# Kernel optimization log

Hardware: AMD Instinct MI355X
Metric: run time of the kernel (lower is better)

Reference implementation:

```python
import jax, jax.numpy as jnp
import numpy as np

B, N, NIN, NH, NOUT = 32, 64, 256, 256, 2
E = N * (N - 1)
BN_EPS = 1e-5


def _xavier(k, fan_in, fan_out):
    return jax.random.normal(k, (fan_in, fan_out), jnp.float32) * np.sqrt(2.0 / (fan_in + fan_out))


def _mlp_params(key, n_in, n_hid, n_out):
    k1, k2 = jax.random.split(key)
    return {
        'w1': _xavier(k1, n_in, n_hid), 'b1': jnp.full((n_hid,), 0.1, jnp.float32),
        'w2': _xavier(k2, n_hid, n_out), 'b2': jnp.full((n_out,), 0.1, jnp.float32),
        'g': jnp.ones((n_out,), jnp.float32), 'beta': jnp.zeros((n_out,), jnp.float32),
    }


def setup_inputs() -> dict:
    key = jax.random.key(0)
    ks = jax.random.split(key, 7)
    inputs = jax.random.normal(ks[0], (B, N, NIN), jnp.float32)
    # fully-connected directed graph w/o self loops: edge e = (send i, recv j), i != j
    idx = np.array([(i, j) for i in range(N) for j in range(N) if i != j], dtype=np.int64)
    rel_send = np.zeros((E, N), np.float32)
    rel_rec = np.zeros((E, N), np.float32)
    rel_send[np.arange(E), idx[:, 0]] = 1.0
    rel_rec[np.arange(E), idx[:, 1]] = 1.0
    out = {'inputs': inputs, 'rel_rec': jnp.asarray(rel_rec), 'rel_send': jnp.asarray(rel_send)}
    for name, (ni, nh, no), k in [('mlp1', (NIN, NH, NH), ks[1]),
                                  ('mlp2', (2 * NH, NH, NH), ks[2]),
                                  ('mlp3', (NH, NH, NH), ks[3]),
                                  ('mlp4', (3 * NH, NH, NH), ks[4])]:
        p = _mlp_params(k, ni, nh, no)
        for pk, pv in p.items():
            out[f'{name}_{pk}'] = pv
    out['fc_w'] = _xavier(ks[5], NH, NOUT)
    out['fc_b'] = jnp.full((NOUT,), 0.1, jnp.float32)
    return out


def _mlp(x, w1, b1, w2, b2, g, beta):
    # Linear -> ELU -> Linear -> ELU -> BatchNorm1d (training-mode batch stats, biased var)
    h = jax.nn.elu(x @ w1 + b1)
    h = jax.nn.elu(h @ w2 + b2)
    mean = h.mean(axis=(0, 1))
    var = h.var(axis=(0, 1))
    return (h - mean) * jax.lax.rsqrt(var + BN_EPS) * g + beta


def reference(inputs, rel_rec, rel_send,
              mlp1_w1, mlp1_b1, mlp1_w2, mlp1_b2, mlp1_g, mlp1_beta,
              mlp2_w1, mlp2_b1, mlp2_w2, mlp2_b2, mlp2_g, mlp2_beta,
              mlp3_w1, mlp3_b1, mlp3_w2, mlp3_b2, mlp3_g, mlp3_beta,
              mlp4_w1, mlp4_b1, mlp4_w2, mlp4_b2, mlp4_g, mlp4_beta,
              fc_w, fc_b):
    x = _mlp(inputs, mlp1_w1, mlp1_b1, mlp1_w2, mlp1_b2, mlp1_g, mlp1_beta)  # [B,N,NH]
    # node2edge: gather sender/receiver node features per edge
    s = jnp.einsum('en,bnh->beh', rel_send, x)
    r = jnp.einsum('en,bnh->beh', rel_rec, x)
    x = jnp.concatenate([s, r], axis=-1)  # [B,E,2*NH]
    x = _mlp(x, mlp2_w1, mlp2_b1, mlp2_w2, mlp2_b2, mlp2_g, mlp2_beta)
    x_skip = x
    # edge2node: scatter-sum incoming edges per node, normalized by N
    inc = jnp.einsum('en,beh->bnh', rel_rec, x) / N
    x = _mlp(inc, mlp3_w1, mlp3_b1, mlp3_w2, mlp3_b2, mlp3_g, mlp3_beta)
    s = jnp.einsum('en,bnh->beh', rel_send, x)
    r = jnp.einsum('en,bnh->beh', rel_rec, x)
    x = jnp.concatenate([s, r, x_skip], axis=-1)  # [B,E,3*NH]
    x = _mlp(x, mlp4_w1, mlp4_b1, mlp4_w2, mlp4_b2, mlp4_g, mlp4_beta)
    return x @ fc_w + fc_b  # [B,E,NOUT]
```

## Files before the change

kernel.cpp:

```cpp
#include <hip/hip_runtime.h>

typedef __bf16 bf16_t;
typedef __bf16 bf16x8 __attribute__((ext_vector_type(8)));
typedef float  f32x4  __attribute__((ext_vector_type(4)));

#define NB    64
#define EB    4032
#define BATCH 32
#define H     256
#define M_EDGE (BATCH*EB)
#define M_NODE (BATCH*NB)
#define T2    4
#define BN_EPS 1e-5f

__device__ __forceinline__ void load_lds16(const void* g, void* l) {
    __builtin_amdgcn_global_load_lds(
        (const __attribute__((address_space(1))) unsigned int*)g,
        (__attribute__((address_space(3))) unsigned int*)l, 16, 0, 0);
}
__device__ __forceinline__ float elu(float v) { return v > 0.f ? v : __expf(v) - 1.f; }

template<bool AF32>
__global__ __launch_bounds__(256)
void fused_mlp(const void* __restrict__ A0v,
               const bf16_t* __restrict__ W1t, const float* __restrict__ b1,
               const bf16_t* __restrict__ W2t, const float* __restrict__ b2,
               bf16_t* __restrict__ out, float* __restrict__ stats)
{
    const int m0 = blockIdx.x * 64;
    const int tid = threadIdx.x, wave = tid >> 6, lane = tid & 63;
    const int l15 = lane & 15, quad = lane >> 4;
    const int row = tid >> 2;
    const int cx8 = (((tid & 3) ^ ((tid >> 3) & 3))) * 8;
    const int sl8 = (tid & 3) * 8;
    const int xq8 = (quad ^ ((l15 >> 1) & 3)) * 8;

    __shared__ bf16_t h1s[64 * 264];
    __shared__ bf16_t Bs[256 * 32];
    __shared__ float  sred[512];

    const bf16_t* A0 = (const bf16_t*)A0v;

    f32x4 acc1[4][4];
#pragma unroll
    for (int t = 0; t < 4; ++t)
#pragma unroll
        for (int u = 0; u < 4; ++u) acc1[t][u] = (f32x4){0.f, 0.f, 0.f, 0.f};

    for (int k0 = 0; k0 < 256; k0 += 32) {
        bf16_t* ldsA = h1s + wave * 512;
        if (AF32) {
            const float* af = (const float*)A0v + (size_t)(m0 + row) * 256 + k0 + cx8;
            float4 lo = *(const float4*)af;
            float4 hi = *(const float4*)(af + 4);
            bf16x8 v;
            v[0]=(bf16_t)lo.x; v[1]=(bf16_t)lo.y; v[2]=(bf16_t)lo.z; v[3]=(bf16_t)lo.w;
            v[4]=(bf16_t)hi.x; v[5]=(bf16_t)hi.y; v[6]=(bf16_t)hi.z; v[7]=(bf16_t)hi.w;
            *(bf16x8*)&h1s[row * 32 + sl8] = v;
        } else {
            load_lds16(A0 + (size_t)(m0 + row) * 256 + k0 + cx8, ldsA);
        }
#pragma unroll
        for (int p = 0; p < 4; ++p)
            load_lds16(W1t + (size_t)(p * 64 + row) * 256 + k0 + cx8,
                       Bs + (p * 256 + wave * 64) * 8);
        __syncthreads();
        bf16x8 afr[4], bfr[4];
#pragma unroll
        for (int t = 0; t < 4; ++t)
            afr[t] = *(const bf16x8*)&h1s[(t * 16 + l15) * 32 + xq8];
#pragma unroll
        for (int u = 0; u < 4; ++u)
            bfr[u] = *(const bf16x8*)&Bs[(wave * 64 + u * 16 + l15) * 32 + xq8];
#pragma unroll
        for (int t = 0; t < 4; ++t)
#pragma unroll
            for (int u = 0; u < 4; ++u)
                acc1[t][u] = __builtin_amdgcn_mfma_f32_16x16x32_bf16(afr[t], bfr[u], acc1[t][u], 0, 0, 0);
        __syncthreads();
    }

#pragma unroll
    for (int u = 0; u < 4; ++u) {
        int   col = wave * 64 + u * 16 + l15;
        float bv  = b1[col];
#pragma unroll
        for (int t = 0; t < 4; ++t)
#pragma unroll
            for (int r = 0; r < 4; ++r)
                h1s[(t * 16 + quad * 4 + r) * 264 + col] = (bf16_t)elu(acc1[t][u][r] + bv);
    }
    sred[tid] = 0.f; sred[256 + tid] = 0.f;
    __syncthreads();

    f32x4 acc2[4][4];
#pragma unroll
    for (int t = 0; t < 4; ++t)
#pragma unroll
        for (int u = 0; u < 4; ++u) acc2[t][u] = (f32x4){0.f, 0.f, 0.f, 0.f};

    for (int k0 = 0; k0 < 256; k0 += 32) {
#pragma unroll
        for (int p = 0; p < 4; ++p)
            load_lds16(W2t + (size_t)(p * 64 + row) * 256 + k0 + cx8,
                       Bs + (p * 256 + wave * 64) * 8);
        __syncthreads();
        bf16x8 afr[4], bfr[4];
#pragma unroll
        for (int t = 0; t < 4; ++t)
            afr[t] = *(const bf16x8*)&h1s[(t * 16 + l15) * 264 + k0 + quad * 8];
#pragma unroll
        for (int u = 0; u < 4; ++u)
            bfr[u] = *(const bf16x8*)&Bs[(wave * 64 + u * 16 + l15) * 32 + xq8];
#pragma unroll
        for (int t = 0; t < 4; ++t)
#pragma unroll
            for (int u = 0; u < 4; ++u)
                acc2[t][u] = __builtin_amdgcn_mfma_f32_16x16x32_bf16(afr[t], bfr[u], acc2[t][u], 0, 0, 0);
        __syncthreads();
    }

#pragma unroll
    for (int u = 0; u < 4; ++u) {
        int   col = wave * 64 + u * 16 + l15;
        float bv  = b2[col];
        float s = 0.f, q = 0.f;
#pragma unroll
        for (int t = 0; t < 4; ++t)
#pragma unroll
            for (int r = 0; r < 4; ++r) {
                float v = elu(acc2[t][u][r] + bv);
                h1s[(t * 16 + quad * 4 + r) * 264 + col] = (bf16_t)v;
                s += v; q += v * v;
            }
        s += __shfl_xor(s, 16); s += __shfl_xor(s, 32);
        q += __shfl_xor(q, 16); q += __shfl_xor(q, 32);
        if (quad == 0) { atomicAdd(&sred[col], s); atomicAdd(&sred[256 + col], q); }
    }
    __syncthreads();
#pragma unroll
    for (int p = 0; p < 8; ++p) {
        int idx = p * 256 + tid;
        int r = idx >> 5, ch = idx & 31;
        *(uint4*)&out[(size_t)(m0 + r) * H + ch * 8] = *(const uint4*)&h1s[r * 264 + ch * 8];
    }
    atomicAdd(&stats[tid],     sred[tid]);
    atomicAdd(&stats[H + tid], sred[256 + tid]);
}

__global__ __launch_bounds__(256)
void node_gemm(const bf16_t* __restrict__ A, const float* __restrict__ statsIn,
               const float* __restrict__ g, const float* __restrict__ beta, float Mcnt,
               const bf16_t* __restrict__ Wt, const float* __restrict__ bias,
               float* __restrict__ out)
{
    const int m0 = blockIdx.x * 64;
    const int nb = blockIdx.y * 256;
    const int tid = threadIdx.x, wave = tid >> 6, lane = tid & 63;
    const int l15 = lane & 15, quad = lane >> 4;
    const int row = tid >> 2;
    const int cx8 = (((tid & 3) ^ ((tid >> 3) & 3))) * 8;
    const int sl8 = (tid & 3) * 8;
    const int xq8 = (quad ^ ((l15 >> 1) & 3)) * 8;
    __shared__ bf16_t As[64 * 32];
    __shared__ bf16_t Bs[256 * 32];
    __shared__ float  ss[512];

    {
        float mean = statsIn[tid] / Mcnt;
        float var  = statsIn[256 + tid] / Mcnt - mean * mean;
        float scl  = g[tid] * rsqrtf(var + BN_EPS);
        ss[tid]       = scl;
        ss[256 + tid] = beta[tid] - mean * scl;
    }
    __syncthreads();

    f32x4 acc[4][4];
#pragma unroll
    for (int t = 0; t < 4; ++t)
#pragma unroll
        for (int u = 0; u < 4; ++u) acc[t][u] = (f32x4){0.f, 0.f, 0.f, 0.f};

    for (int k0 = 0; k0 < 256; k0 += 32) {
        {
            int kc = k0 + cx8;
            bf16x8 v = *(const bf16x8*)(A + (size_t)(m0 + row) * 256 + kc);
            bf16x8 w;
#pragma unroll
            for (int j = 0; j < 8; ++j)
                w[j] = (bf16_t)((float)v[j] * ss[kc + j] + ss[256 + kc + j]);
            *(bf16x8*)&As[row * 32 + sl8] = w;
        }
#pragma unroll
        for (int p = 0; p < 4; ++p)
            load_lds16(Wt + (size_t)(nb + p * 64 + row) * 256 + k0 + cx8,
                       Bs + (p * 256 + wave * 64) * 8);
        __syncthreads();
        bf16x8 afr[4], bfr[4];
#pragma unroll
        for (int t = 0; t < 4; ++t)
            afr[t] = *(const bf16x8*)&As[(t * 16 + l15) * 32 + xq8];
#pragma unroll
        for (int u = 0; u < 4; ++u)
            bfr[u] = *(const bf16x8*)&Bs[(wave * 64 + u * 16 + l15) * 32 + xq8];
#pragma unroll
        for (int t = 0; t < 4; ++t)
#pragma unroll
            for (int u = 0; u < 4; ++u)
                acc[t][u] = __builtin_amdgcn_mfma_f32_16x16x32_bf16(afr[t], bfr[u], acc[t][u], 0, 0, 0);
        __syncthreads();
    }
#pragma unroll
    for (int u = 0; u < 4; ++u) {
        int col = nb + wave * 64 + u * 16 + l15;
        float bv = bias[col];
#pragma unroll
        for (int t = 0; t < 4; ++t)
#pragma unroll
            for (int r = 0; r < 4; ++r)
                out[(size_t)(m0 + t * 16 + quad * 4 + r) * 512 + col] = acc[t][u][r] + bv;
    }
}

__global__ __launch_bounds__(256, 2)
void m2_kernel(const float* __restrict__ PQ, const bf16_t* __restrict__ W2t,
               const float* __restrict__ b2, bf16_t* __restrict__ out,
               float* __restrict__ stats)
{
    const int tile0 = blockIdx.x * T2;
    const int tid = threadIdx.x, wave = tid >> 6, lane = tid & 63;
    const int l15 = lane & 15, quad = lane >> 4;

    __shared__ bf16_t Abuf[2][64 * 264];
    __shared__ float  sred[512];

    bf16x8 Breg[32];
#pragma unroll
    for (int ks = 0; ks < 8; ++ks)
#pragma unroll
        for (int u = 0; u < 4; ++u) {
            int col = wave * 64 + u * 16 + l15;
            Breg[ks * 4 + u] = *(const bf16x8*)(W2t + (size_t)col * 256 + ks * 32 + quad * 8);
        }
    sred[tid] = 0.f; sred[256 + tid] = 0.f;

    auto computeA = [&](int t, int b) {
        int row = tid >> 2;
        int m = (tile0 + t) * 64 + row;
        int bb = m / EB, e = m - bb * EB;
        int sn = e / (NB - 1), rr = e - sn * (NB - 1);
        int rc = rr + (rr >= sn ? 1 : 0);
        const float* Prow = PQ + (size_t)(bb * NB + sn) * 512;
        const float* Qrow = PQ + (size_t)(bb * NB + rc) * 512 + 256;
        int c0 = (tid & 3) * 64;
#pragma unroll
        for (int j = 0; j < 8; ++j) {
            int c = c0 + j * 8;
            float4 p0 = *(const float4*)(Prow + c);
            float4 p1 = *(const float4*)(Prow + c + 4);
            float4 q0 = *(const float4*)(Qrow + c);
            float4 q1 = *(const float4*)(Qrow + c + 4);
            bf16x8 v;
            v[0]=(bf16_t)elu(p0.x+q0.x); v[1]=(bf16_t)elu(p0.y+q0.y);
            v[2]=(bf16_t)elu(p0.z+q0.z); v[3]=(bf16_t)elu(p0.w+q0.w);
            v[4]=(bf16_t)elu(p1.x+q1.x); v[5]=(bf16_t)elu(p1.y+q1.y);
            v[6]=(bf16_t)elu(p1.z+q1.z); v[7]=(bf16_t)elu(p1.w+q1.w);
            *(bf16x8*)&Abuf[b][row * 264 + c] = v;
        }
    };

    computeA(0, 0);
    __syncthreads();

    for (int t = 0; t < T2; ++t) {
        const int cur = t & 1, nxt = cur ^ 1;
        if (t + 1 < T2) computeA(t + 1, nxt);

        f32x4 acc[4][4];
#pragma unroll
        for (int a = 0; a < 4; ++a)
#pragma unroll
            for (int u = 0; u < 4; ++u) acc[a][u] = (f32x4){0.f, 0.f, 0.f, 0.f};
#pragma unroll
        for (int ks = 0; ks < 8; ++ks) {
            bf16x8 afr[4];
#pragma unroll
            for (int a = 0; a < 4; ++a)
                afr[a] = *(const bf16x8*)&Abuf[cur][(a * 16 + l15) * 264 + ks * 32 + quad * 8];
#pragma unroll
            for (int a = 0; a < 4; ++a)
#pragma unroll
                for (int u = 0; u < 4; ++u)
                    acc[a][u] = __builtin_amdgcn_mfma_f32_16x16x32_bf16(afr[a], Breg[ks * 4 + u], acc[a][u], 0, 0, 0);
        }
        __syncthreads();

#pragma unroll
        for (int u = 0; u < 4; ++u) {
            int   col = wave * 64 + u * 16 + l15;
            float bv  = b2[col];
            float s = 0.f, q = 0.f;
#pragma unroll
            for (int a = 0; a < 4; ++a)
#pragma unroll
                for (int r = 0; r < 4; ++r) {
                    float v = elu(acc[a][u][r] + bv);
                    Abuf[cur][(a * 16 + quad * 4 + r) * 264 + col] = (bf16_t)v;
                    s += v; q += v * v;
                }
            s += __shfl_xor(s, 16); s += __shfl_xor(s, 32);
            q += __shfl_xor(q, 16); q += __shfl_xor(q, 32);
            if (quad == 0) { atomicAdd(&sred[col], s); atomicAdd(&sred[256 + col], q); }
        }
        __syncthreads();

        size_t m0 = (size_t)(tile0 + t) * 64;
#pragma unroll
        for (int p = 0; p < 8; ++p) {
            int idx = p * 256 + tid;
            int r = idx >> 5, ch = idx & 31;
            *(uint4*)&out[(m0 + r) * H + ch * 8] = *(const uint4*)&Abuf[cur][r * 264 + ch * 8];
        }
        __syncthreads();
    }
    atomicAdd(&stats[tid],     sred[tid]);
    atomicAdd(&stats[H + tid], sred[256 + tid]);
}

__global__ __launch_bounds__(256)
void m4_kernel(const bf16_t* __restrict__ h2, const bf16_t* __restrict__ Wskt,
               const float* __restrict__ RS, const bf16_t* __restrict__ W2t,
               const float* __restrict__ b2, bf16_t* __restrict__ out,
               float* __restrict__ stats)
{
    const int m0 = blockIdx.x * 64;
    const int tid = threadIdx.x, wave = tid >> 6, lane = tid & 63;
    const int l15 = lane & 15, quad = lane >> 4;
    const int row = tid >> 2;
    const int cx8 = (((tid & 3) ^ ((tid >> 3) & 3))) * 8;
    const int xq8 = (quad ^ ((l15 >> 1) & 3)) * 8;

    __shared__ bf16_t h1s[64 * 264];
    __shared__ bf16_t Bs[256 * 32];
    __shared__ float  sred[512];
    __shared__ int    sndN[64], rcvN[64];

    if (tid < 64) {
        int m = m0 + tid, bb = m / EB, e = m - bb * EB;
        int sn = e / (NB - 1), rr = e - sn * (NB - 1);
        int rc = rr + (rr >= sn ? 1 : 0);
        sndN[tid] = bb * NB + sn;
        rcvN[tid] = bb * NB + rc;
    }

    f32x4 acc1[4][4];
#pragma unroll
    for (int t = 0; t < 4; ++t)
#pragma unroll
        for (int u = 0; u < 4; ++u) acc1[t][u] = (f32x4){0.f, 0.f, 0.f, 0.f};

    for (int k0 = 0; k0 < 256; k0 += 32) {
        load_lds16(h2 + (size_t)(m0 + row) * 256 + k0 + cx8, h1s + wave * 512);
#pragma unroll
        for (int p = 0; p < 4; ++p)
            load_lds16(Wskt + (size_t)(p * 64 + row) * 256 + k0 + cx8,
                       Bs + (p * 256 + wave * 64) * 8);
        __syncthreads();
        bf16x8 afr[4], bfr[4];
#pragma unroll
        for (int t = 0; t < 4; ++t)
            afr[t] = *(const bf16x8*)&h1s[(t * 16 + l15) * 32 + xq8];
#pragma unroll
        for (int u = 0; u < 4; ++u)
            bfr[u] = *(const bf16x8*)&Bs[(wave * 64 + u * 16 + l15) * 32 + xq8];
#pragma unroll
        for (int t = 0; t < 4; ++t)
#pragma unroll
            for (int u = 0; u < 4; ++u)
                acc1[t][u] = __builtin_amdgcn_mfma_f32_16x16x32_bf16(afr[t], bfr[u], acc1[t][u], 0, 0, 0);
        __syncthreads();
    }

#pragma unroll
    for (int u = 0; u < 4; ++u) {
        int col = wave * 64 + u * 16 + l15;
#pragma unroll
        for (int t = 0; t < 4; ++t)
#pragma unroll
            for (int r = 0; r < 4; ++r)
                h1s[(t * 16 + quad * 4 + r) * 264 + col] = (bf16_t)acc1[t][u][r];
    }
    sred[tid] = 0.f; sred[256 + tid] = 0.f;
    __syncthreads();

    {
        const float* Srow = RS + (size_t)sndN[row] * 512;
        const float* Rrow = RS + (size_t)rcvN[row] * 512 + 256;
        int c0 = (tid & 3) * 64;
#pragma unroll
        for (int j = 0; j < 8; ++j) {
            int c = c0 + j * 8;
            bf16x8 h = *(const bf16x8*)&h1s[row * 264 + c];
            float4 s0 = *(const float4*)(Srow + c);
            float4 s1 = *(const float4*)(Srow + c + 4);
            float4 r0 = *(const float4*)(Rrow + c);
            float4 r1 = *(const float4*)(Rrow + c + 4);
            bf16x8 v;
            v[0]=(bf16_t)elu((float)h[0]+s0.x+r0.x); v[1]=(bf16_t)elu((float)h[1]+s0.y+r0.y);
            v[2]=(bf16_t)elu((float)h[2]+s0.z+r0.z); v[3]=(bf16_t)elu((float)h[3]+s0.w+r0.w);
            v[4]=(bf16_t)elu((float)h[4]+s1.x+r1.x); v[5]=(bf16_t)elu((float)h[5]+s1.y+r1.y);
            v[6]=(bf16_t)elu((float)h[6]+s1.z+r1.z); v[7]=(bf16_t)elu((float)h[7]+s1.w+r1.w);
            *(bf16x8*)&h1s[row * 264 + c] = v;
        }
    }
    __syncthreads();

    f32x4 acc2[4][4];
#pragma unroll
    for (int t = 0; t < 4; ++t)
#pragma unroll
        for (int u = 0; u < 4; ++u) acc2[t][u] = (f32x4){0.f, 0.f, 0.f, 0.f};

    for (int k0 = 0; k0 < 256; k0 += 32) {
#pragma unroll
        for (int p = 0; p < 4; ++p)
            load_lds16(W2t + (size_t)(p * 64 + row) * 256 + k0 + cx8,
                       Bs + (p * 256 + wave * 64) * 8);
        __syncthreads();
        bf16x8 afr[4], bfr[4];
#pragma unroll
        for (int t = 0; t < 4; ++t)
            afr[t] = *(const bf16x8*)&h1s[(t * 16 + l15) * 264 + k0 + quad * 8];
#pragma unroll
        for (int u = 0; u < 4; ++u)
            bfr[u] = *(const bf16x8*)&Bs[(wave * 64 + u * 16 + l15) * 32 + xq8];
#pragma unroll
        for (int t = 0; t < 4; ++t)
#pragma unroll
            for (int u = 0; u < 4; ++u)
                acc2[t][u] = __builtin_amdgcn_mfma_f32_16x16x32_bf16(afr[t], bfr[u], acc2[t][u], 0, 0, 0);
        __syncthreads();
    }

#pragma unroll
    for (int u = 0; u < 4; ++u) {
        int   col = wave * 64 + u * 16 + l15;
        float bv  = b2[col];
        float s = 0.f, q = 0.f;
#pragma unroll
        for (int t = 0; t < 4; ++t)
#pragma unroll
            for (int r = 0; r < 4; ++r) {
                float v = elu(acc2[t][u][r] + bv);
                h1s[(t * 16 + quad * 4 + r) * 264 + col] = (bf16_t)v;
                s += v; q += v * v;
            }
        s += __shfl_xor(s, 16); s += __shfl_xor(s, 32);
        q += __shfl_xor(q, 16); q += __shfl_xor(q, 32);
        if (quad == 0) { atomicAdd(&sred[col], s); atomicAdd(&sred[256 + col], q); }
    }
    __syncthreads();
#pragma unroll
    for (int p = 0; p < 8; ++p) {
        int idx = p * 256 + tid;
        int r = idx >> 5, ch = idx & 31;
        *(uint4*)&out[(size_t)(m0 + r) * H + ch * 8] = *(const uint4*)&h1s[r * 264 + ch * 8];
    }
    atomicAdd(&stats[tid],     sred[tid]);
    atomicAdd(&stats[H + tid], sred[256 + tid]);
}

__global__ void prep(const float* __restrict__ w1a, bf16_t* __restrict__ wt1a,
                     const float* __restrict__ w1b, bf16_t* __restrict__ wt1b,
                     const float* __restrict__ w2b, bf16_t* __restrict__ wt2b,
                     const float* __restrict__ w3a, bf16_t* __restrict__ wt3a,
                     const float* __restrict__ w3b, bf16_t* __restrict__ wt3b,
                     const float* __restrict__ w4b, bf16_t* __restrict__ wt4b,
                     const float* __restrict__ w2a, bf16_t* __restrict__ wtpq,
                     const float* __restrict__ w4a, bf16_t* __restrict__ wtrs,
                     const float* __restrict__ b2a, float* __restrict__ biasPQ,
                     float* __restrict__ stats)
{
    int blk = blockIdx.x, tid = threadIdx.x;
    if (blk < 1536) {
        int grp = blk >> 8, lb = blk & 255;
        const float* w; bf16_t* wt;
        switch (grp) {
            case 0: w = w1a; wt = wt1a; break;
            case 1: w = w1b; wt = wt1b; break;
            case 2: w = w2b; wt = wt2b; break;
            case 3: w = w3a; wt = wt3a; break;
            case 4: w = w3b; wt = wt3b; break;
            default: w = w4b; wt = wt4b; break;
        }
        int idx = lb * 256 + tid;
        int k = idx >> 8, n = idx & 255;
        wt[n * 256 + k] = (bf16_t)w[idx];
    } else if (blk < 2560) {
        int lb = blk - 1536;
        const float* w = (lb < 512) ? w2a : w4a;
        bf16_t* wt = (lb < 512) ? wtpq : wtrs;
        int c = lb & 511, k = tid;
        float v = (c < 256) ? w[k * 256 + c] : w[(256 + k) * 256 + (c - 256)];
        wt[c * 256 + k] = (bf16_t)v;
    } else if (blk == 2560) {
        biasPQ[tid] = b2a[tid];
        biasPQ[256 + tid] = 0.f;
    } else {
        for (int j = 0; j < 8; ++j) stats[j * 256 + tid] = 0.f;
    }
}

__global__ void prep2(const float* __restrict__ w4a, const float* __restrict__ stats2,
                      const float* __restrict__ g2, const float* __restrict__ be2,
                      const float* __restrict__ b4a, bf16_t* __restrict__ wt,
                      float* __restrict__ bias)
{
    __shared__ float sh2s[256];
    int blk = blockIdx.x, tid = threadIdx.x;
    float mean = stats2[tid] / (float)M_EDGE;
    float var  = stats2[256 + tid] / (float)M_EDGE - mean * mean;
    float scl  = g2[tid] * rsqrtf(var + BN_EPS);
    if (blk < 256) {
        wt[blk * 256 + tid] = (bf16_t)(w4a[(512 + tid) * 256 + blk] * scl);
    } else {
        sh2s[tid] = be2[tid] - mean * scl;
        __syncthreads();
        float acc = 0.f;
        for (int k = 0; k < 256; ++k)
            acc += sh2s[k] * w4a[(512 + k) * 256 + tid];
        bias[tid] = b4a[tid] + acc;
        bias[256 + tid] = 0.f;
    }
}

__global__ void edge2node(const bf16_t* __restrict__ x2, const float* __restrict__ stats2,
                          const float* __restrict__ g2, const float* __restrict__ be2,
                          bf16_t* __restrict__ inc)
{
    int bn = blockIdx.x, bb = bn >> 6, n = bn & 63;
    int g = threadIdx.x >> 5, t = threadIdx.x & 31;
    __shared__ float part[8][256];
    __shared__ float ss[512];
    {
        int c = threadIdx.x;
        float mean = stats2[c] / (float)M_EDGE;
        float var  = stats2[256 + c] / (float)M_EDGE - mean * mean;
        float scl  = g2[c] * rsqrtf(var + BN_EPS);
        ss[c]       = scl;
        ss[256 + c] = be2[c] - mean * scl;
    }
    const bf16_t* base = x2 + (size_t)bb * EB * H;
    float a[8] = {0.f,0.f,0.f,0.f,0.f,0.f,0.f,0.f};
    for (int i = g; i < NB; i += 8) {
        if (i == n) continue;
        int e = i * (NB - 1) + n - (n > i ? 1 : 0);
        bf16x8 v = *(const bf16x8*)&base[(size_t)e * H + t * 8];
#pragma unroll
        for (int j = 0; j < 8; ++j) a[j] += (float)v[j];
    }
#pragma unroll
    for (int j = 0; j < 8; ++j) part[g][t * 8 + j] = a[j];
    __syncthreads();
    int c = threadIdx.x;
    float s = 0.f;
#pragma unroll
    for (int g2i = 0; g2i < 8; ++g2i) s += part[g2i][c];
    inc[(size_t)bn * H + c] = (bf16_t)(s * (1.f / 64.f) * ss[c] + ss[256 + c] * (63.f / 64.f));
}

__global__ void fc_kernel(const bf16_t* __restrict__ x4, const float* __restrict__ stats4,
                          const float* __restrict__ g4, const float* __restrict__ be4,
                          const float* __restrict__ fcw, const float* __restrict__ fcb,
                          float* __restrict__ out)
{
    __shared__ float ss[512];
    {
        int c = threadIdx.x;
        float mean = stats4[c] / (float)M_EDGE;
        float var  = stats4[256 + c] / (float)M_EDGE - mean * mean;
        float scl  = g4[c] * rsqrtf(var + BN_EPS);
        ss[c]       = scl;
        ss[256 + c] = be4[c] - mean * scl;
    }
    __syncthreads();
    int row  = blockIdx.x * 8 + (threadIdx.x >> 5);
    int t    = threadIdx.x & 31;
    bf16x8 v8 = *(const bf16x8*)(x4 + (size_t)row * H + t * 8);
    float s0 = 0.f, s1 = 0.f;
#pragma unroll
    for (int j = 0; j < 8; ++j) {
        int c = t * 8 + j;
        float v = (float)v8[j] * ss[c] + ss[256 + c];
        s0 += v * fcw[c * 2];
        s1 += v * fcw[c * 2 + 1];
    }
#pragma unroll
    for (int off = 16; off; off >>= 1) {
        s0 += __shfl_down(s0, off, 32);
        s1 += __shfl_down(s1, off, 32);
    }
    if (t == 0) {
        out[(size_t)row * 2]     = s0 + fcb[0];
        out[(size_t)row * 2 + 1] = s1 + fcb[1];
    }
}

extern "C" void kernel_launch(void* const* d_in, const int* in_sizes, int n_in,
                              void* d_out, int out_size, void* d_ws, size_t ws_size,
                              hipStream_t stream)
{
    (void)in_sizes; (void)n_in; (void)out_size; (void)ws_size;
    const float* inp = (const float*)d_in[0];
    const float* w1a = (const float*)d_in[3];  const float* b1a = (const float*)d_in[4];
    const float* w1b = (const float*)d_in[5];  const float* b1b = (const float*)d_in[6];
    const float* g1  = (const float*)d_in[7];  const float* be1 = (const float*)d_in[8];
    const float* w2a = (const float*)d_in[9];  const float* b2a = (const float*)d_in[10];
    const float* w2b = (const float*)d_in[11]; const float* b2b = (const float*)d_in[12];
    const float* g2  = (const float*)d_in[13]; const float* be2 = (const float*)d_in[14];
    const float* w3a = (const float*)d_in[15]; const float* b3a = (const float*)d_in[16];
    const float* w3b = (const float*)d_in[17]; const float* b3b = (const float*)d_in[18];
    const float* g3  = (const float*)d_in[19]; const float* be3 = (const float*)d_in[20];
    const float* w4a = (const float*)d_in[21]; const float* b4a = (const float*)d_in[22];
    const float* w4b = (const float*)d_in[23]; const float* b4b = (const float*)d_in[24];
    const float* g4  = (const float*)d_in[25]; const float* be4 = (const float*)d_in[26];
    const float* fcw = (const float*)d_in[27]; const float* fcb = (const float*)d_in[28];

    char* p = (char*)d_ws;
    auto alloc = [&](size_t nbytes) { char* r = p; p += (nbytes + 255) & ~(size_t)255; return r; };

    bf16_t* wt1a = (bf16_t*)alloc(256 * 256 * 2);
    bf16_t* wt1b = (bf16_t*)alloc(256 * 256 * 2);
    bf16_t* wt2b = (bf16_t*)alloc(256 * 256 * 2);
    bf16_t* wt3a = (bf16_t*)alloc(256 * 256 * 2);
    bf16_t* wt3b = (bf16_t*)alloc(256 * 256 * 2);
    bf16_t* wt4b = (bf16_t*)alloc(256 * 256 * 2);
    bf16_t* wtpq = (bf16_t*)alloc(512 * 256 * 2);
    bf16_t* wtrs = (bf16_t*)alloc(512 * 256 * 2);
    bf16_t* wtsk = (bf16_t*)alloc(256 * 256 * 2);
    float*  biasPQ = (float*)alloc(512 * sizeof(float));
    float*  biasRS = (float*)alloc(512 * sizeof(float));
    float*  stats  = (float*)alloc(4 * 512 * sizeof(float));
    bf16_t* x1   = (bf16_t*)alloc((size_t)M_NODE * H * 2);
    bf16_t* incb = (bf16_t*)alloc((size_t)M_NODE * H * 2);
    bf16_t* x3   = (bf16_t*)alloc((size_t)M_NODE * H * 2);
    float*  PQ   = (float*)alloc((size_t)M_NODE * 512 * sizeof(float));
    float*  RS   = (float*)alloc((size_t)M_NODE * 512 * sizeof(float));
    bf16_t* h2   = (bf16_t*)alloc((size_t)M_EDGE * H * 2);
    bf16_t* h4   = (bf16_t*)alloc((size_t)M_EDGE * H * 2);

    prep<<<2562, 256, 0, stream>>>(w1a, wt1a, w1b, wt1b, w2b, wt2b, w3a, wt3a,
                                   w3b, wt3b, w4b, wt4b, w2a, wtpq, w4a, wtrs,
                                   b2a, biasPQ, stats);

    fused_mlp<true ><<<M_NODE / 64, 256, 0, stream>>>(inp, wt1a, b1a, wt1b, b1b, x1, stats + 0);

    { dim3 g(M_NODE / 64, 2);
      node_gemm<<<g, 256, 0, stream>>>(x1, stats + 0, g1, be1, (float)M_NODE, wtpq, biasPQ, PQ); }

    m2_kernel<<<M_EDGE / (64 * T2), 256, 0, stream>>>(PQ, wt2b, b2b, h2, stats + 512);

    edge2node<<<M_NODE, 256, 0, stream>>>(h2, stats + 512, g2, be2, incb);
    fused_mlp<false><<<M_NODE / 64, 256, 0, stream>>>(incb, wt3a, b3a, wt3b, b3b, x3, stats + 1024);

    prep2<<<257, 256, 0, stream>>>(w4a, stats + 512, g2, be2, b4a, wtsk, biasRS);
    { dim3 g(M_NODE / 64, 2);
      node_gemm<<<g, 256, 0, stream>>>(x3, stats + 1024, g3, be3, (float)M_NODE, wtrs, biasRS, RS); }

    m4_kernel<<<M_EDGE / 64, 256, 0, stream>>>(h2, wtsk, RS, wt4b, b4b, h4, stats + 1536);

    fc_kernel<<<M_EDGE / 8, 256, 0, stream>>>(h4, stats + 1536, g4, be4, fcw, fcb, (float*)d_out);
}
```

Baseline: 374.5 us.

## Make m4 kernel persistent over 4 tiles with register-resident weights

Result: slower. 408.8 us (+9.2%).

```diff
diff --git a/kernel.cpp b/kernel.cpp
--- a/kernel.cpp
+++ b/kernel.cpp
@@ -11,6 +11,7 @@
 #define M_EDGE (BATCH*EB)
 #define M_NODE (BATCH*NB)
 #define T2    4
+#define T4    4
 #define BN_EPS 1e-5f
 
 __device__ __forceinline__ void load_lds16(const void* g, void* l) {
@@ -327,144 +328,151 @@
     atomicAdd(&stats[H + tid], sred[256 + tid]);
 }
 
-__global__ __launch_bounds__(256)
+__global__ __launch_bounds__(256, 1)
 void m4_kernel(const bf16_t* __restrict__ h2, const bf16_t* __restrict__ Wskt,
                const float* __restrict__ RS, const bf16_t* __restrict__ W2t,
                const float* __restrict__ b2, bf16_t* __restrict__ out,
                float* __restrict__ stats)
 {
-    const int m0 = blockIdx.x * 64;
+    const int tile0 = blockIdx.x * T4;
     const int tid = threadIdx.x, wave = tid >> 6, lane = tid & 63;
     const int l15 = lane & 15, quad = lane >> 4;
-    const int row = tid >> 2;
-    const int cx8 = (((tid & 3) ^ ((tid >> 3) & 3))) * 8;
-    const int xq8 = (quad ^ ((l15 >> 1) & 3)) * 8;
-
-    __shared__ bf16_t h1s[64 * 264];
-    __shared__ bf16_t Bs[256 * 32];
+
+    __shared__ bf16_t Abuf[2][64 * 264];
     __shared__ float  sred[512];
-    __shared__ int    sndN[64], rcvN[64];
-
-    if (tid < 64) {
-        int m = m0 + tid, bb = m / EB, e = m - bb * EB;
-        int sn = e / (NB - 1), rr = e - sn * (NB - 1);
-        int rc = rr + (rr >= sn ? 1 : 0);
-        sndN[tid] = bb * NB + sn;
-        rcvN[tid] = bb * NB + rc;
-    }
-
-    f32x4 acc1[4][4];
-#pragma unroll
-    for (int t = 0; t < 4; ++t)
-#pragma unroll
-        for (int u = 0; u < 4; ++u) acc1[t][u] = (f32x4){0.f, 0.f, 0.f, 0.f};
-
-    for (int k0 = 0; k0 < 256; k0 += 32) {
-        load_lds16(h2 + (size_t)(m0 + row) * 256 + k0 + cx8, h1s + wave * 512);
-#pragma unroll
-        for (int p = 0; p < 4; ++p)
-            load_lds16(Wskt + (size_t)(p * 64 + row) * 256 + k0 + cx8,
-                       Bs + (p * 256 + wave * 64) * 8);
-        __syncthreads();
-        bf16x8 afr[4], bfr[4];
-#pragma unroll
-        for (int t = 0; t < 4; ++t)
-            afr[t] = *(const bf16x8*)&h1s[(t * 16 + l15) * 32 + xq8];
-#pragma unroll
-        for (int u = 0; u < 4; ++u)
-            bfr[u] = *(const bf16x8*)&Bs[(wave * 64 + u * 16 + l15) * 32 + xq8];
-#pragma unroll
-        for (int t = 0; t < 4; ++t)
-#pragma unroll
-            for (int u = 0; u < 4; ++u)
-                acc1[t][u] = __builtin_amdgcn_mfma_f32_16x16x32_bf16(afr[t], bfr[u], acc1[t][u], 0, 0, 0);
-        __syncthreads();
-    }
-
-#pragma unroll
-    for (int u = 0; u < 4; ++u) {
-        int col = wave * 64 + u * 16 + l15;
-#pragma unroll
-        for (int t = 0; t < 4; ++t)
-#pragma unroll
-            for (int r = 0; r < 4; ++r)
-                h1s[(t * 16 + quad * 4 + r) * 264 + col] = (bf16_t)acc1[t][u][r];
-    }
+
+    bf16x8 B1r[32], B2r[32];
+#pragma unroll
+    for (int ks = 0; ks < 8; ++ks)
+#pragma unroll
+        for (int u = 0; u < 4; ++u) {
+            int col = wave * 64 + u * 16 + l15;
+            B1r[ks * 4 + u] = *(const bf16x8*)(Wskt + (size_t)col * 256 + ks * 32 + quad * 8);
+            B2r[ks * 4 + u] = *(const bf16x8*)(W2t  + (size_t)col * 256 + ks * 32 + quad * 8);
+        }
     sred[tid] = 0.f; sred[256 + tid] = 0.f;
-    __syncthreads();
-
-    {
-        const float* Srow = RS + (size_t)sndN[row] * 512;
-        const float* Rrow = RS + (size_t)rcvN[row] * 512 + 256;
+
+    auto stageA = [&](int t, int b) {
+        int row = tid >> 2;
+        const bf16_t* src = h2 + ((size_t)(tile0 + t) * 64 + row) * 256;
         int c0 = (tid & 3) * 64;
 #pragma unroll
         for (int j = 0; j < 8; ++j) {
             int c = c0 + j * 8;
-            bf16x8 h = *(const bf16x8*)&h1s[row * 264 + c];
-            float4 s0 = *(const float4*)(Srow + c);
-            float4 s1 = *(const float4*)(Srow + c + 4);
-            float4 r0 = *(const float4*)(Rrow + c);
-            float4 r1 = *(const float4*)(Rrow + c + 4);
-            bf16x8 v;
-            v[0]=(bf16_t)elu((float)h[0]+s0.x+r0.x); v[1]=(bf16_t)elu((float)h[1]+s0.y+r0.y);
-            v[2]=(bf16_t)elu((float)h[2]+s0.z+r0.z); v[3]=(bf16_t)elu((float)h[3]+s0.w+r0.w);
-            v[4]=(bf16_t)elu((float)h[4]+s1.x+r1.x); v[5]=(bf16_t)elu((float)h[5]+s1.y+r1.y);
-            v[6]=(bf16_t)elu((float)h[6]+s1.z+r1.z); v[7]=(bf16_t)elu((float)h[7]+s1.w+r1.w);
-            *(bf16x8*)&h1s[row * 264 + c] = v;
-        }
-    }
+            *(bf16x8*)&Abuf[b][row * 264 + c] = *(const bf16x8*)(src + c);
+        }
+    };
+
+    stageA(0, 0);
     __syncthreads();
 
-    f32x4 acc2[4][4];
-#pragma unroll
-    for (int t = 0; t < 4; ++t)
-#pragma unroll
-        for (int u = 0; u < 4; ++u) acc2[t][u] = (f32x4){0.f, 0.f, 0.f, 0.f};
-
-    for (int k0 = 0; k0 < 256; k0 += 32) {
-#pragma unroll
-        for (int p = 0; p < 4; ++p)
-            load_lds16(W2t + (size_t)(p * 64 + row) * 256 + k0 + cx8,
-                       Bs + (p * 256 + wave * 64) * 8);
-        __syncthreads();
-        bf16x8 afr[4], bfr[4];
-#pragma unroll
-        for (int t = 0; t < 4; ++t)
-            afr[t] = *(const bf16x8*)&h1s[(t * 16 + l15) * 264 + k0 + quad * 8];
-#pragma unroll
-        for (int u = 0; u < 4; ++u)
-            bfr[u] = *(const bf16x8*)&Bs[(wave * 64 + u * 16 + l15) * 32 + xq8];
-#pragma unroll
-        for (int t = 0; t < 4; ++t)
-#pragma unroll
-            for (int u = 0; u < 4; ++u)
-                acc2[t][u] = __builtin_amdgcn_mfma_f32_16x16x32_bf16(afr[t], bfr[u], acc2[t][u], 0, 0, 0);
-        __syncthreads();
-    }
-
-#pragma unroll
-    for (int u = 0; u < 4; ++u) {
-        int   col = wave * 64 + u * 16 + l15;
-        float bv  = b2[col];
-        float s = 0.f, q = 0.f;
-#pragma unroll
-        for (int t = 0; t < 4; ++t)
-#pragma unroll
-            for (int r = 0; r < 4; ++r) {
-                float v = elu(acc2[t][u][r] + bv);
-                h1s[(t * 16 + quad * 4 + r) * 264 + col] = (bf16_t)v;
-                s += v; q += v * v;
+    for (int t = 0; t < T4; ++t) {
+        const int cur = t & 1, nxt = cur ^ 1;
+        if (t + 1 < T4) stageA(t + 1, nxt);
+
+        f32x4 acc[4][4];
+#pragma unroll
+        for (int a = 0; a < 4; ++a)
+#pragma unroll
+            for (int u = 0; u < 4; ++u) acc[a][u] = (f32x4){0.f, 0.f, 0.f, 0.f};
+
+#pragma unroll
+        for (int ks = 0; ks < 8; ++ks) {
+            bf16x8 afr[4];
+#pragma unroll
+            for (int a = 0; a < 4; ++a)
+                afr[a] = *(const bf16x8*)&Abuf[cur][(a * 16 + l15) * 264 + ks * 32 + quad * 8];
+#pragma unroll
+            for (int a = 0; a < 4; ++a)
+#pragma unroll
+                for (int u = 0; u < 4; ++u)
+                    acc[a][u] = __builtin_amdgcn_mfma_f32_16x16x32_bf16(afr[a], B1r[ks * 4 + u], acc[a][u], 0, 0, 0);
+        }
+        __syncthreads();
+
+#pragma unroll
+        for (int u = 0; u < 4; ++u) {
+            int col = wave * 64 + u * 16 + l15;
+#pragma unroll
+            for (int a = 0; a < 4; ++a)
+#pragma unroll
+                for (int r = 0; r < 4; ++r)
+                    Abuf[cur][(a * 16 + quad * 4 + r) * 264 + col] = (bf16_t)acc[a][u][r];
+        }
+        __syncthreads();
+
+        {
+            int row = tid >> 2;
+            int m = (tile0 + t) * 64 + row;
+            int bb = m / EB, e = m - bb * EB;
+            int sn = e / (NB - 1), rr = e - sn * (NB - 1);
+            int rc = rr + (rr >= sn ? 1 : 0);
+            const float* Srow = RS + (size_t)(bb * NB + sn) * 512;
+            const float* Rrow = RS + (size_t)(bb * NB + rc) * 512 + 256;
+            int c0 = (tid & 3) * 64;
+#pragma unroll
+            for (int j = 0; j < 8; ++j) {
+                int c = c0 + j * 8;
+                bf16x8 h = *(const bf16x8*)&Abuf[cur][row * 264 + c];
+                float4 s0 = *(const float4*)(Srow + c);
+                float4 s1 = *(const float4*)(Srow + c + 4);
+                float4 r0 = *(const float4*)(Rrow + c);
+                float4 r1 = *(const float4*)(Rrow + c + 4);
+                bf16x8 v;
+                v[0]=(bf16_t)elu((float)h[0]+s0.x+r0.x); v[1]=(bf16_t)elu((float)h[1]+s0.y+r0.y);
+                v[2]=(bf16_t)elu((float)h[2]+s0.z+r0.z); v[3]=(bf16_t)elu((float)h[3]+s0.w+r0.w);
+                v[4]=(bf16_t)elu((float)h[4]+s1.x+r1.x); v[5]=(bf16_t)elu((float)h[5]+s1.y+r1.y);
+                v[6]=(bf16_t)elu((float)h[6]+s1.z+r1.z); v[7]=(bf16_t)elu((float)h[7]+s1.w+r1.w);
+                *(bf16x8*)&Abuf[cur][row * 264 + c] = v;
             }
-        s += __shfl_xor(s, 16); s += __shfl_xor(s, 32);
-        q += __shfl_xor(q, 16); q += __shfl_xor(q, 32);
-        if (quad == 0) { atomicAdd(&sred[col], s); atomicAdd(&sred[256 + col], q); }
-    }
-    __syncthreads();
-#pragma unroll
-    for (int p = 0; p < 8; ++p) {
-        int idx = p * 256 + tid;
-        int r = idx >> 5, ch = idx & 31;
-        *(uint4*)&out[(size_t)(m0 + r) * H + ch * 8] = *(const uint4*)&h1s[r * 264 + ch * 8];
+        }
+        __syncthreads();
+
+#pragma unroll
+        for (int a = 0; a < 4; ++a)
+#pragma unroll
+            for (int u = 0; u < 4; ++u) acc[a][u] = (f32x4){0.f, 0.f, 0.f, 0.f};
+#pragma unroll
+        for (int ks = 0; ks < 8; ++ks) {
+            bf16x8 afr[4];
+#pragma unroll
+            for (int a = 0; a < 4; ++a)
+                afr[a] = *(const bf16x8*)&Abuf[cur][(a * 16 + l15) * 264 + ks * 32 + quad * 8];
+#pragma unroll
+            for (int a = 0; a < 4; ++a)
+#pragma unroll
+                for (int u = 0; u < 4; ++u)
+                    acc[a][u] = __builtin_amdgcn_mfma_f32_16x16x32_bf16(afr[a], B2r[ks * 4 + u], acc[a][u], 0, 0, 0);
+        }
+        __syncthreads();
+
+#pragma unroll
+        for (int u = 0; u < 4; ++u) {
+            int   col = wave * 64 + u * 16 + l15;
+            float bv  = b2[col];
+            float s = 0.f, q = 0.f;
+#pragma unroll
+            for (int a = 0; a < 4; ++a)
+#pragma unroll
+                for (int r = 0; r < 4; ++r) {
+                    float v = elu(acc[a][u][r] + bv);
+                    Abuf[cur][(a * 16 + quad * 4 + r) * 264 + col] = (bf16_t)v;
+                    s += v; q += v * v;
+                }
+            s += __shfl_xor(s, 16); s += __shfl_xor(s, 32);
+            q += __shfl_xor(q, 16); q += __shfl_xor(q, 32);
+            if (quad == 0) { atomicAdd(&sred[col], s); atomicAdd(&sred[256 + col], q); }
+        }
+        __syncthreads();
+
+        size_t m0 = (size_t)(tile0 + t) * 64;
+#pragma unroll
+        for (int p = 0; p < 8; ++p) {
+            int idx = p * 256 + tid;
+            int r = idx >> 5, ch = idx & 31;
+            *(uint4*)&out[(m0 + r) * H + ch * 8] = *(const uint4*)&Abuf[cur][r * 264 + ch * 8];
+        }
+        __syncthreads();
     }
     atomicAdd(&stats[tid],     sred[tid]);
     atomicAdd(&stats[H + tid], sred[256 + tid]);
@@ -667,7 +675,7 @@
     { dim3 g(M_NODE / 64, 2);
       node_gemm<<<g, 256, 0, stream>>>(x3, stats + 1024, g3, be3, (float)M_NODE, wtrs, biasRS, RS); }
 
-    m4_kernel<<<M_EDGE / 64, 256, 0, stream>>>(h2, wtsk, RS, wt4b, b4b, h4, stats + 1536);
+    m4_kernel<<<M_EDGE / (64 * T4), 256, 0, stream>>>(h2, wtsk, RS, wt4b, b4b, h4, stats + 1536);
 
     fc_kernel<<<M_EDGE / 8, 256, 0, stream>>>(h4, stats + 1536, g4, be4, fcw, fcb, (float*)d_out);
 }
```
